# Kernel tuning notes

Measured on AMD Instinct MI355X. Metric: run time of the kernel, lower is better.

The kernel has to match this reference:

```python
import jax, jax.numpy as jnp
import numpy as np

N = 100_000          # nodes
E = 1_600_000        # directed edges (before self-loops)
IN_DIM, H1, H2, H3 = 128, 64, 64, 64
NEG_SLOPE = 0.2      # PyG GATConv default


def setup_inputs() -> dict:
    key = jax.random.key(0)
    ks = jax.random.split(key, 20)

    def glorot(k, shape):
        fan = shape[0] + shape[-1] if len(shape) > 1 else 1 + shape[0]
        return jax.random.normal(k, shape, jnp.float32) * np.float32(np.sqrt(2.0 / fan))

    inp = {
        "x": jax.random.normal(ks[0], (N, IN_DIM), jnp.float32),
        "edge_index": jax.random.randint(ks[1], (2, E), 0, N, jnp.int32),
        "W1": glorot(ks[2], (IN_DIM, H1)), "a1s": glorot(ks[3], (H1,)), "a1d": glorot(ks[4], (H1,)), "b1": jnp.zeros((H1,), jnp.float32),
        "W2": glorot(ks[5], (H1, H2)),     "a2s": glorot(ks[6], (H2,)), "a2d": glorot(ks[7], (H2,)), "b2": jnp.zeros((H2,), jnp.float32),
        "W3": glorot(ks[8], (H2, H3)),     "a3s": glorot(ks[9], (H3,)), "a3d": glorot(ks[10], (H3,)), "b3": jnp.zeros((H3,), jnp.float32),
        "Wl": glorot(ks[11], (H3, 1)),     "bl": jnp.zeros((1,), jnp.float32),
    }
    return inp


def _gat_layer(x, src, dst, W, a_src, a_dst, b):
    # x: [N, Fin]; src/dst: [E'] (self-loops included)
    h = x @ W                              # [N, Fout]
    alpha_s = h @ a_src                    # [N]
    alpha_d = h @ a_dst                    # [N]
    e = jax.nn.leaky_relu(alpha_s[src] + alpha_d[dst], NEG_SLOPE)  # [E']
    # segment softmax over edges grouped by destination node
    m = jax.ops.segment_max(e, dst, num_segments=N)
    p = jnp.exp(e - m[dst])
    s = jax.ops.segment_sum(p, dst, num_segments=N)
    alpha = p / (s[dst] + 1e-16)           # [E']
    out = jax.ops.segment_sum(alpha[:, None] * h[src], dst, num_segments=N)  # [N, Fout]
    return out + b


def reference(x, edge_index, W1, a1s, a1d, b1, W2, a2s, a2d, b2, W3, a3s, a3d, b3, Wl, bl):
    # add self-loops (PyG GATConv default add_self_loops=True)
    loops = jnp.arange(N, dtype=edge_index.dtype)
    src = jnp.concatenate([edge_index[0], loops])
    dst = jnp.concatenate([edge_index[1], loops])

    h = jax.nn.relu(_gat_layer(x, src, dst, W1, a1s, a1d, b1))   # dropout is identity in eval
    h = jax.nn.relu(_gat_layer(h, src, dst, W2, a2s, a2d, b2))
    h = jax.nn.relu(_gat_layer(h, src, dst, W3, a3s, a3d, b3))
    return jax.nn.sigmoid(h @ Wl + bl)      # [N, 1]
```

## Files before the change

kernel.cpp:

```cpp
#include <hip/hip_runtime.h>
#include <hip/hip_bf16.h>
#include <math.h>

#define BSH 8
#define MAXBK 512
#define PCHUNK 4096

__device__ __forceinline__ float wave_reduce_sum(float v) {
  #pragma unroll
  for (int off = 32; off; off >>= 1) v += __shfl_xor(v, off);
  return v;
}
__device__ __forceinline__ float half_reduce_max(float v) {
  #pragma unroll
  for (int off = 16; off; off >>= 1) v = fmaxf(v, __shfl_xor(v, off));
  return v;
}
__device__ __forceinline__ float half_reduce_sum(float v) {
  #pragma unroll
  for (int off = 16; off; off >>= 1) v += __shfl_xor(v, off);
  return v;
}

__device__ __forceinline__ unsigned f2bf(float f) {
  unsigned u = __float_as_uint(f);
  return (u + 0x7fffu + ((u >> 16) & 1u)) >> 16;
}

__device__ __forceinline__ void async_copy16(const float* gsrc, float* ldst) {
  __builtin_amdgcn_global_load_lds(
      (const __attribute__((address_space(1))) void*)gsrc,
      (__attribute__((address_space(3))) void*)ldst, 16, 0, 0);
}

__device__ __forceinline__ void wave0_excl_scan(unsigned* arr, unsigned* out, int n, int t) {
  if (t < 64) {
    unsigned carry = 0;
    for (int c = 0; c < n / 64; c++) {
      unsigned v = arr[c * 64 + t];
      unsigned s = v;
      #pragma unroll
      for (int off = 1; off < 64; off <<= 1) {
        unsigned u = __shfl_up(s, off);
        if ((t & 63) >= off) s += u;
      }
      out[c * 64 + t] = s - v + carry;
      carry += __shfl(s, 63);
    }
  }
}


__global__ __launch_bounds__(256) void k_bhist(const int* __restrict__ ei,
                                               unsigned* __restrict__ gbucket,
                                               int E, int EE, int nbk) {
  __shared__ unsigned hist[MAXBK];
  int t = threadIdx.x;
  for (int i = t; i < nbk; i += 256) hist[i] = 0;
  __syncthreads();
  for (int e = blockIdx.x * 256 + t; e < EE; e += gridDim.x * 256) {
    int d = (e < E) ? ei[E + e] : (e - E);
    atomicAdd(&hist[d >> BSH], 1u);
  }
  __syncthreads();
  for (int i = t; i < nbk; i += 256)
    if (hist[i]) atomicAdd(&gbucket[i], hist[i]);
}

__global__ __launch_bounds__(256) void k_bscan(const unsigned* __restrict__ gbucket,
                                               unsigned* __restrict__ bbase,
                                               unsigned* __restrict__ bfill,
                                               int nbk, int EE) {
  __shared__ unsigned arr[MAXBK], exc[MAXBK];
  int t = threadIdx.x;
  for (int i = t; i < MAXBK; i += 256) arr[i] = (i < nbk) ? gbucket[i] : 0u;
  __syncthreads();
  wave0_excl_scan(arr, exc, MAXBK, t);
  __syncthreads();
  for (int i = t; i < nbk; i += 256) { bbase[i] = exc[i]; bfill[i] = exc[i]; }
  if (t == 0) bbase[nbk] = (unsigned)EE;
}

__global__ __launch_bounds__(256) void k_part(const int* __restrict__ ei,
                                              unsigned* __restrict__ bfill,
                                              uint2* __restrict__ part,
                                              int E, int EE) {
  __shared__ uint2 stage[PCHUNK];
  __shared__ unsigned lcnt[MAXBK], lexcl[MAXBK], lbase[MAXBK];
  int t = threadIdx.x;
  int base = blockIdx.x * PCHUNK;
  int cnt = EE - base; if (cnt > PCHUNK) cnt = PCHUNK;
  for (int i = t; i < MAXBK; i += 256) lcnt[i] = 0;
  __syncthreads();

  uint2 ed[16]; unsigned loc[16];
  #pragma unroll
  for (int i = 0; i < 16; i++) {
    int e = base + i * 256 + t;
    if (e < EE) {
      int s, d;
      if (e < E) { s = ei[e]; d = ei[E + e]; } else { s = e - E; d = s; }
      ed[i] = make_uint2((unsigned)s, (unsigned)d);
      loc[i] = atomicAdd(&lcnt[(unsigned)d >> BSH], 1u);
    }
  }
  __syncthreads();
  wave0_excl_scan(lcnt, lexcl, MAXBK, t);
  __syncthreads();
  for (int i = t; i < MAXBK; i += 256) {
    unsigned c = lcnt[i];
    lbase[i] = c ? atomicAdd(&bfill[i], c) : 0u;
  }
  __syncthreads();
  #pragma unroll
  for (int i = 0; i < 16; i++) {
    int e = base + i * 256 + t;
    if (e < EE) stage[lexcl[ed[i].y >> BSH] + loc[i]] = ed[i];
  }
  __syncthreads();
  for (int i = t; i < cnt; i += 256) {
    uint2 v = stage[i];
    unsigned b = v.y >> BSH;
    part[lbase[b] + ((unsigned)i - lexcl[b])] = v;
  }
}

__global__ __launch_bounds__(256) void k_bcsr(const uint2* __restrict__ part,
                                              const unsigned* __restrict__ bbase,
                                              int* __restrict__ rowptr,
                                              int* __restrict__ csr_src,
                                              int Nn, int nbk) {
  __shared__ unsigned sdeg[256], sexcl[256], sfill[256];
  int t = threadIdx.x, b = blockIdx.x;
  int e0 = (int)bbase[b], e1 = (int)bbase[b + 1];
  sdeg[t] = 0; sfill[t] = 0;
  __syncthreads();
  for (int j = e0 + t; j < e1; j += 256)
    atomicAdd(&sdeg[part[j].y & 255u], 1u);
  __syncthreads();
  wave0_excl_scan(sdeg, sexcl, 256, t);
  __syncthreads();
  int node = (b << BSH) + t;
  if (node < Nn) rowptr[node] = e0 + (int)sexcl[t];
  if (b == nbk - 1 && t == 0) rowptr[Nn] = e1;
  for (int j = e0 + t; j < e1; j += 256) {
    uint2 v = part[j];
    unsigned dl = v.y & 255u;
    unsigned k = atomicAdd(&sfill[dl], 1u);
    csr_src[e0 + (int)sexcl[dl] + (int)k] = (int)v.x;
  }
}


template <int FIN>
__device__ __forceinline__ void stage_tile(const float* __restrict__ x, float* xs,
                                           int tile, int wid, int lane) {
  const size_t base = (size_t)tile * (32 * FIN);
  #pragma unroll
  for (int i = 0; i < FIN / 32; i++) {
    int chunk = wid * (FIN / 32) + i;
    async_copy16(x + base + chunk * 256 + lane * 4, xs + chunk * 256);
  }
}

#define FMA2(av, wr) \
  acc0[r] = fmaf(av, wreg[wr].x, acc0[r]); \
  acc1[r] = fmaf(av, wreg[wr].y, acc1[r]);

template <int FIN>
__global__ __launch_bounds__(256) void k_gemm5(
    const float* __restrict__ x, const float* __restrict__ W,
    const float* __restrict__ avs, const float* __restrict__ avd,
    unsigned* __restrict__ h, float* __restrict__ as_out, float* __restrict__ ad_out,
    int Nn, int ntiles) {
  __shared__ float Wl[FIN * 64];
  __shared__ float xs[2][32 * FIN];
  int t = threadIdx.x, lane = t & 63, wid = t >> 6;
  int fl = lane & 31, rh = lane >> 5;

  #pragma unroll
  for (int i = 0; i < FIN / 16; i++)
    ((float4*)Wl)[i * 256 + t] = ((const float4*)W)[i * 256 + t];
  float2 As2 = *(const float2*)&avs[2 * fl];
  float2 Ad2 = *(const float2*)&avd[2 * fl];

  int tile = blockIdx.x;
  if (tile >= ntiles) return;
  stage_tile<FIN>(x, xs[0], tile, wid, lane);
  __syncthreads();
  int buf = 0;

  while (tile < ntiles) {
    int nxt = tile + gridDim.x;
    if (nxt < ntiles) stage_tile<FIN>(x, xs[buf ^ 1], nxt, wid, lane);

    float acc0[4], acc1[4];
    #pragma unroll
    for (int r = 0; r < 4; r++) { acc0[r] = 0.f; acc1[r] = 0.f; }
    const float* xw = &xs[buf][(wid * 8 + rh * 4) * FIN];
    const float2* wcol = (const float2*)&Wl[2 * fl];

    #pragma unroll 1
    for (int kb = 0; kb < FIN; kb += 16) {
      float2 wreg[16];
      #pragma unroll
      for (int k = 0; k < 16; k++) wreg[k] = wcol[(kb + k) * 32];
      #pragma unroll
      for (int r = 0; r < 4; r++) {
        const float4* xr = (const float4*)(xw + r * FIN + kb);
        float4 a0 = xr[0], a1 = xr[1], a2 = xr[2], a3 = xr[3];
        FMA2(a0.x, 0)  FMA2(a0.y, 1)  FMA2(a0.z, 2)  FMA2(a0.w, 3)
        FMA2(a1.x, 4)  FMA2(a1.y, 5)  FMA2(a1.z, 6)  FMA2(a1.w, 7)
        FMA2(a2.x, 8)  FMA2(a2.y, 9)  FMA2(a2.z, 10) FMA2(a2.w, 11)
        FMA2(a3.x, 12) FMA2(a3.y, 13) FMA2(a3.z, 14) FMA2(a3.w, 15)
      }
    }

    int row0 = tile * 32 + wid * 8 + rh * 4;
    #pragma unroll
    for (int r = 0; r < 4; r++) {
      int row = row0 + r;
      bool ok = row < Nn;
      if (ok) {
        unsigned pk = (f2bf(acc1[r]) << 16) | f2bf(acc0[r]);
        h[(size_t)row * 32 + fl] = pk;
      }
      float vs = acc0[r] * As2.x + acc1[r] * As2.y;
      float vd = acc0[r] * Ad2.x + acc1[r] * Ad2.y;
      #pragma unroll
      for (int off = 16; off; off >>= 1) {
        vs += __shfl_xor(vs, off);
        vd += __shfl_xor(vd, off);
      }
      if (ok && fl == 0) { as_out[row] = vs; ad_out[row] = vd; }
    }

    __syncthreads();
    buf ^= 1;
    tile = nxt;
  }
}


template <int FINAL>
__global__ __launch_bounds__(256) void k_agg6(
    const int* __restrict__ rowptr, const int* __restrict__ csr_src,
    const unsigned* __restrict__ hp, const float* __restrict__ as_,
    const float* __restrict__ ad_, const float* __restrict__ bias,
    float* __restrict__ out, const float* __restrict__ Wlin,
    const float* __restrict__ blin, float* __restrict__ fout, int Nn) {
  __shared__ float2 psbuf[4][2][32];
  int t = threadIdx.x, lane = t & 63, wid = t >> 6;
  int fl = lane & 31, hh = lane >> 5;
  int n = blockIdx.x * 8 + wid * 2 + hh;
  bool valid = n < Nn;
  int nn = valid ? n : (Nn - 1);
  int r0 = rowptr[nn], r1 = rowptr[nn + 1];
  int deg = valid ? (r1 - r0) : 0;
  float ad = ad_[nn];
  float acc0 = 0.f, acc1 = 0.f;
  float inv;

  if (deg <= 32) {
    int src = (fl < deg) ? csr_src[r0 + fl] : 0;
    float e = (fl < deg) ? (as_[src] + ad) : -3.0e38f;
    e = (e >= 0.f) ? e : 0.2f * e;
    float m = half_reduce_max(e);
    float p = (fl < deg) ? __expf(e - m) : 0.f;
    inv = 1.f / (half_reduce_sum(p) + 1e-16f);
    psbuf[wid][hh][fl] = make_float2(p, __int_as_float(src));

    float b0 = 0.f, b1 = 0.f;
    int jj = 0;
    for (; jj + 2 <= deg; jj += 2) {
      float2 ps0 = psbuf[wid][hh][jj];
      float2 ps1 = psbuf[wid][hh][jj + 1];
      unsigned v0 = hp[(size_t)__float_as_int(ps0.y) * 32 + fl];
      unsigned v1 = hp[(size_t)__float_as_int(ps1.y) * 32 + fl];
      acc0 = fmaf(ps0.x, __uint_as_float(v0 << 16), acc0);
      acc1 = fmaf(ps0.x, __uint_as_float(v0 & 0xffff0000u), acc1);
      b0 = fmaf(ps1.x, __uint_as_float(v1 << 16), b0);
      b1 = fmaf(ps1.x, __uint_as_float(v1 & 0xffff0000u), b1);
    }
    if (jj < deg) {
      float2 ps0 = psbuf[wid][hh][jj];
      unsigned v0 = hp[(size_t)__float_as_int(ps0.y) * 32 + fl];
      acc0 = fmaf(ps0.x, __uint_as_float(v0 << 16), acc0);
      acc1 = fmaf(ps0.x, __uint_as_float(v0 & 0xffff0000u), acc1);
    }
    acc0 = (acc0 + b0) * inv;
    acc1 = (acc1 + b1) * inv;
  } else {
    float m = -3.0e38f;
    for (int j = r0 + fl; j < r1; j += 32) {
      float e = as_[csr_src[j]] + ad;
      e = (e >= 0.f) ? e : 0.2f * e;
      m = fmaxf(m, e);
    }
    m = half_reduce_max(m);
    float ssum = 0.f;
    for (int j = r0; j < r1; ++j) {
      int src = csr_src[j];
      float e = as_[src] + ad;
      e = (e >= 0.f) ? e : 0.2f * e;
      float p = __expf(e - m);
      ssum += p;
      unsigned v = hp[(size_t)src * 32 + fl];
      acc0 = fmaf(p, __uint_as_float(v << 16), acc0);
      acc1 = fmaf(p, __uint_as_float(v & 0xffff0000u), acc1);
    }
    float inv2 = 1.f / (ssum + 1e-16f);
    acc0 *= inv2;
    acc1 *= inv2;
  }

  float2 bi = ((const float2*)bias)[fl];
  float o0 = fmaxf(acc0 + bi.x, 0.f);
  float o1 = fmaxf(acc1 + bi.y, 0.f);
  if (FINAL) {
    float2 wl = ((const float2*)Wlin)[fl];
    float rv = half_reduce_sum(o0 * wl.x + o1 * wl.y);
    if (valid && fl == 0) {
      float z = rv + blin[0];
      fout[n] = 1.f / (1.f + __expf(-z));
    }
  } else {
    if (valid) ((float2*)out)[(size_t)n * 32 + fl] = make_float2(o0, o1);
  }
}

extern "C" void kernel_launch(void* const* d_in, const int* in_sizes, int n_in,
                              void* d_out, int out_size, void* d_ws, size_t ws_size,
                              hipStream_t stream) {
  const float* x   = (const float*)d_in[0];
  const int*   ei  = (const int*)d_in[1];
  const float* W1  = (const float*)d_in[2];
  const float* a1s = (const float*)d_in[3];
  const float* a1d = (const float*)d_in[4];
  const float* b1  = (const float*)d_in[5];
  const float* W2  = (const float*)d_in[6];
  const float* a2s = (const float*)d_in[7];
  const float* a2d = (const float*)d_in[8];
  const float* b2  = (const float*)d_in[9];
  const float* W3  = (const float*)d_in[10];
  const float* a3s = (const float*)d_in[11];
  const float* a3d = (const float*)d_in[12];
  const float* b3  = (const float*)d_in[13];
  const float* Wl  = (const float*)d_in[14];
  const float* bl  = (const float*)d_in[15];

  const int N  = in_sizes[0] / 128;
  const int E  = in_sizes[1] / 2;
  const int EE = E + N;
  const int nbk = (N + 255) >> 8;

  char* p = (char*)d_ws;
  auto alloc = [&](size_t bytes) { char* r = p; p += (bytes + 255) & ~(size_t)255; return r; };
  unsigned* gbucket = (unsigned*)alloc((size_t)MAXBK * 4);
  unsigned* bbase   = (unsigned*)alloc((size_t)(MAXBK + 1) * 4);
  unsigned* bfill   = (unsigned*)alloc((size_t)MAXBK * 4);
  int*      rowptr  = (int*)alloc((size_t)(N + 1) * 4);
  int*      csr_src = (int*)alloc((size_t)EE * 4);
  unsigned* hbuf    = (unsigned*)alloc((size_t)N * 64 * 2);
  float*    obuf    = (float*)alloc((size_t)N * 64 * 4);
  float*    as_     = (float*)alloc((size_t)N * 4);
  float*    ad_     = (float*)alloc((size_t)N * 4);

  uint2* part = (uint2*)obuf;

  hipMemsetAsync(gbucket, 0, (size_t)MAXBK * 4, stream);

  k_bhist<<<256, 256, 0, stream>>>(ei, gbucket, E, EE, nbk);
  k_bscan<<<1, 256, 0, stream>>>(gbucket, bbase, bfill, nbk, EE);
  k_part<<<(EE + PCHUNK - 1) / PCHUNK, 256, 0, stream>>>(ei, bfill, part, E, EE);
  k_bcsr<<<nbk, 256, 0, stream>>>(part, bbase, rowptr, csr_src, N, nbk);

  int ntiles = (N + 31) / 32;
  int g1 = ntiles < 512 ? ntiles : 512;
  int g2 = ntiles < 1024 ? ntiles : 1024;
  int nb = (N + 7) / 8;

  k_gemm5<128><<<g1, 256, 0, stream>>>(x, W1, a1s, a1d, hbuf, as_, ad_, N, ntiles);
  k_agg6<0><<<nb, 256, 0, stream>>>(rowptr, csr_src, hbuf, as_, ad_, b1, obuf,
                                    nullptr, nullptr, nullptr, N);
  k_gemm5<64><<<g2, 256, 0, stream>>>(obuf, W2, a2s, a2d, hbuf, as_, ad_, N, ntiles);
  k_agg6<0><<<nb, 256, 0, stream>>>(rowptr, csr_src, hbuf, as_, ad_, b2, obuf,
                                    nullptr, nullptr, nullptr, N);
  k_gemm5<64><<<g2, 256, 0, stream>>>(obuf, W3, a3s, a3d, hbuf, as_, ad_, N, ntiles);
  k_agg6<1><<<nb, 256, 0, stream>>>(rowptr, csr_src, hbuf, as_, ad_, b3, nullptr,
                                    Wl, bl, (float*)d_out, N);
}
```

Baseline: 295.6 us.

## Use bf16 MFMA for GAT projections and store intermediate activations as bf16

Replaces the fp32 FMA projection GEMM with a kernel using 32x32x16 bf16 MFMA, with the weights pre-packed into MFMA fragment layout by a small prep kernel. Input tiles are staged into LDS with an XOR swizzle, and 128 rows are handled per block without a persistent loop. Aggregation now writes hidden activations as packed bf16, which halves the traffic read by the next GEMM. The intended saving is the ALU cost of the GEMMs and the memory traffic between layers. The cost is lower precision on the inputs and activations, and the loss of the double-buffered pipelining.

```diff
diff --git a/kernel.cpp b/kernel.cpp
--- a/kernel.cpp
+++ b/kernel.cpp
@@ -6,11 +6,9 @@
 #define MAXBK 512
 #define PCHUNK 4096
 
-__device__ __forceinline__ float wave_reduce_sum(float v) {
-  #pragma unroll
-  for (int off = 32; off; off >>= 1) v += __shfl_xor(v, off);
-  return v;
-}
+typedef __attribute__((ext_vector_type(8)))  short short8;
+typedef __attribute__((ext_vector_type(16))) float f32x16;
+
 __device__ __forceinline__ float half_reduce_max(float v) {
   #pragma unroll
   for (int off = 16; off; off >>= 1) v = fmaxf(v, __shfl_xor(v, off));
@@ -27,7 +25,7 @@
   return (u + 0x7fffu + ((u >> 16) & 1u)) >> 16;
 }
 
-__device__ __forceinline__ void async_copy16(const float* gsrc, float* ldst) {
+__device__ __forceinline__ void async_copy16(const void* gsrc, void* ldst) {
   __builtin_amdgcn_global_load_lds(
       (const __attribute__((address_space(1))) void*)gsrc,
       (__attribute__((address_space(3))) void*)ldst, 16, 0, 0);
@@ -152,102 +150,111 @@
 }
 
 
-template <int FIN>
-__device__ __forceinline__ void stage_tile(const float* __restrict__ x, float* xs,
-                                           int tile, int wid, int lane) {
-  const size_t base = (size_t)tile * (32 * FIN);
-  #pragma unroll
-  for (int i = 0; i < FIN / 32; i++) {
-    int chunk = wid * (FIN / 32) + i;
-    async_copy16(x + base + chunk * 256 + lane * 4, xs + chunk * 256);
-  }
-}
-
-#define FMA2(av, wr) \
-  acc0[r] = fmaf(av, wreg[wr].x, acc0[r]); \
-  acc1[r] = fmaf(av, wreg[wr].y, acc1[r]);
-
-template <int FIN>
-__global__ __launch_bounds__(256) void k_gemm5(
-    const float* __restrict__ x, const float* __restrict__ W,
+__global__ __launch_bounds__(256) void k_wprep(const float* __restrict__ W1,
+                                               const float* __restrict__ W2,
+                                               const float* __restrict__ W3,
+                                               short8* __restrict__ wf) {
+  int idx = blockIdx.x * 256 + threadIdx.x;
+  if (idx >= 2048) return;
+  int g = idx >> 6, l = idx & 63;
+  const float* W; int s, t;
+  if (g < 16)      { W = W1; s = g >> 1;        t = g & 1; }
+  else if (g < 24) { W = W2; s = (g - 16) >> 1; t = g & 1; }
+  else             { W = W3; s = (g - 24) >> 1; t = g & 1; }
+  int of = t * 32 + (l & 31);
+  int k0 = s * 16 + (l >> 5) * 8;
+  short8 v;
+  #pragma unroll
+  for (int e = 0; e < 8; e++) v[e] = (short)f2bf(W[(k0 + e) * 64 + of]);
+  wf[idx] = v;
+}
+
+
+template <int K, bool F32IN>
+__global__ __launch_bounds__(256) void k_gemm7(
+    const void* __restrict__ xin, const short8* __restrict__ wf,
     const float* __restrict__ avs, const float* __restrict__ avd,
-    unsigned* __restrict__ h, float* __restrict__ as_out, float* __restrict__ ad_out,
-    int Nn, int ntiles) {
-  __shared__ float Wl[FIN * 64];
-  __shared__ float xs[2][32 * FIN];
+    unsigned* __restrict__ h, float* __restrict__ as_out,
+    float* __restrict__ ad_out, int Nn) {
+  constexpr int NS = K / 16;
+  constexpr int RB = F32IN ? K * 4 : K * 2;
+  constexpr int RSH = F32IN ? (K == 128 ? 9 : 8) : (K == 128 ? 8 : 7);
+  __shared__ __align__(16) char xs_raw[128 * RB];
   int t = threadIdx.x, lane = t & 63, wid = t >> 6;
-  int fl = lane & 31, rh = lane >> 5;
-
-  #pragma unroll
-  for (int i = 0; i < FIN / 16; i++)
-    ((float4*)Wl)[i * 256 + t] = ((const float4*)W)[i * 256 + t];
-  float2 As2 = *(const float2*)&avs[2 * fl];
-  float2 Ad2 = *(const float2*)&avd[2 * fl];
-
-  int tile = blockIdx.x;
-  if (tile >= ntiles) return;
-  stage_tile<FIN>(x, xs[0], tile, wid, lane);
-  __syncthreads();
-  int buf = 0;
-
-  while (tile < ntiles) {
-    int nxt = tile + gridDim.x;
-    if (nxt < ntiles) stage_tile<FIN>(x, xs[buf ^ 1], nxt, wid, lane);
-
-    float acc0[4], acc1[4];
-    #pragma unroll
-    for (int r = 0; r < 4; r++) { acc0[r] = 0.f; acc1[r] = 0.f; }
-    const float* xw = &xs[buf][(wid * 8 + rh * 4) * FIN];
-    const float2* wcol = (const float2*)&Wl[2 * fl];
-
-    #pragma unroll 1
-    for (int kb = 0; kb < FIN; kb += 16) {
-      float2 wreg[16];
-      #pragma unroll
-      for (int k = 0; k < 16; k++) wreg[k] = wcol[(kb + k) * 32];
-      #pragma unroll
-      for (int r = 0; r < 4; r++) {
-        const float4* xr = (const float4*)(xw + r * FIN + kb);
-        float4 a0 = xr[0], a1 = xr[1], a2 = xr[2], a3 = xr[3];
-        FMA2(a0.x, 0)  FMA2(a0.y, 1)  FMA2(a0.z, 2)  FMA2(a0.w, 3)
-        FMA2(a1.x, 4)  FMA2(a1.y, 5)  FMA2(a1.z, 6)  FMA2(a1.w, 7)
-        FMA2(a2.x, 8)  FMA2(a2.y, 9)  FMA2(a2.z, 10) FMA2(a2.w, 11)
-        FMA2(a3.x, 12) FMA2(a3.y, 13) FMA2(a3.z, 14) FMA2(a3.w, 15)
-      }
-    }
-
-    int row0 = tile * 32 + wid * 8 + rh * 4;
-    #pragma unroll
-    for (int r = 0; r < 4; r++) {
-      int row = row0 + r;
-      bool ok = row < Nn;
-      if (ok) {
-        unsigned pk = (f2bf(acc1[r]) << 16) | f2bf(acc0[r]);
-        h[(size_t)row * 32 + fl] = pk;
-      }
-      float vs = acc0[r] * As2.x + acc1[r] * As2.y;
-      float vd = acc0[r] * Ad2.x + acc1[r] * Ad2.y;
-      #pragma unroll
-      for (int off = 16; off; off >>= 1) {
-        vs += __shfl_xor(vs, off);
-        vd += __shfl_xor(vd, off);
-      }
-      if (ok && fl == 0) { as_out[row] = vs; ad_out[row] = vd; }
-    }
-
-    __syncthreads();
-    buf ^= 1;
-    tile = nxt;
-  }
+  int l31 = lane & 31, hi = lane >> 5;
+
+  short8 wa[NS * 2];
+  #pragma unroll
+  for (int i = 0; i < NS * 2; i++) wa[i] = wf[i * 64 + lane];
+
+  int tile0 = blockIdx.x * 128;
+  const char* xg = (const char*)xin;
+  constexpr int CH = (128 * RB) / (256 * 16);
+  #pragma unroll
+  for (int i = 0; i < CH; i++) {
+    int off = (i * 256 + t) * 16;
+    int row = off >> RSH;
+    int inrow = off & (RB - 1);
+    long grow = (long)tile0 + row;
+    if (grow > (long)Nn - 1) grow = Nn - 1;
+    async_copy16(xg + grow * RB + (inrow ^ ((row & 7) << 4)), xs_raw + off);
+  }
+  __syncthreads();
+
+  f32x16 acc0 = {0,0,0,0,0,0,0,0,0,0,0,0,0,0,0,0};
+  f32x16 acc1 = {0,0,0,0,0,0,0,0,0,0,0,0,0,0,0,0};
+  int rowl = wid * 32 + l31;
+  int swz = (rowl & 7) << 4;
+
+  #pragma unroll
+  for (int s = 0; s < NS; s++) {
+    short8 bf;
+    if constexpr (F32IN) {
+      int ph = (rowl * RB + s * 64 + hi * 32) ^ swz;
+      float4 fA = *(const float4*)(xs_raw + ph);
+      float4 fB = *(const float4*)(xs_raw + (ph ^ 16));
+      bf[0] = (short)f2bf(fA.x); bf[1] = (short)f2bf(fA.y);
+      bf[2] = (short)f2bf(fA.z); bf[3] = (short)f2bf(fA.w);
+      bf[4] = (short)f2bf(fB.x); bf[5] = (short)f2bf(fB.y);
+      bf[6] = (short)f2bf(fB.z); bf[7] = (short)f2bf(fB.w);
+    } else {
+      int ph = (rowl * RB + s * 32 + hi * 16) ^ swz;
+      bf = *(const short8*)(xs_raw + ph);
+    }
+    acc0 = __builtin_amdgcn_mfma_f32_32x32x16_bf16(wa[2 * s], bf, acc0, 0, 0, 0);
+    acc1 = __builtin_amdgcn_mfma_f32_32x32x16_bf16(wa[2 * s + 1], bf, acc1, 0, 0, 0);
+  }
+
+  int xrow = tile0 + rowl;
+  bool ok = xrow < Nn;
+  float asp = 0.f, adp = 0.f;
+  #pragma unroll
+  for (int r = 0; r < 16; r += 2) {
+    int rof = (r & 3) + 8 * (r >> 2);
+    int of0 = rof + 4 * hi;
+    if (ok) {
+      h[(size_t)xrow * 32 + (of0 >> 1)] =
+          (f2bf(acc0[r + 1]) << 16) | f2bf(acc0[r]);
+      h[(size_t)xrow * 32 + 16 + (of0 >> 1)] =
+          (f2bf(acc1[r + 1]) << 16) | f2bf(acc1[r]);
+    }
+    asp += acc0[r] * avs[of0] + acc0[r + 1] * avs[of0 + 1]
+         + acc1[r] * avs[of0 + 32] + acc1[r + 1] * avs[of0 + 33];
+    adp += acc0[r] * avd[of0] + acc0[r + 1] * avd[of0 + 1]
+         + acc1[r] * avd[of0 + 32] + acc1[r + 1] * avd[of0 + 33];
+  }
+  asp += __shfl_xor(asp, 32);
+  adp += __shfl_xor(adp, 32);
+  if (ok && hi == 0) { as_out[xrow] = asp; ad_out[xrow] = adp; }
 }
 
 
 template <int FINAL>
-__global__ __launch_bounds__(256) void k_agg6(
+__global__ __launch_bounds__(256) void k_agg7(
     const int* __restrict__ rowptr, const int* __restrict__ csr_src,
     const unsigned* __restrict__ hp, const float* __restrict__ as_,
     const float* __restrict__ ad_, const float* __restrict__ bias,
-    float* __restrict__ out, const float* __restrict__ Wlin,
+    unsigned* __restrict__ out, const float* __restrict__ Wlin,
     const float* __restrict__ blin, float* __restrict__ fout, int Nn) {
   __shared__ float2 psbuf[4][2][32];
   int t = threadIdx.x, lane = t & 63, wid = t >> 6;
@@ -259,7 +266,6 @@
   int deg = valid ? (r1 - r0) : 0;
   float ad = ad_[nn];
   float acc0 = 0.f, acc1 = 0.f;
-  float inv;
 
   if (deg <= 32) {
     int src = (fl < deg) ? csr_src[r0 + fl] : 0;
@@ -267,7 +273,7 @@
     e = (e >= 0.f) ? e : 0.2f * e;
     float m = half_reduce_max(e);
     float p = (fl < deg) ? __expf(e - m) : 0.f;
-    inv = 1.f / (half_reduce_sum(p) + 1e-16f);
+    float inv = 1.f / (half_reduce_sum(p) + 1e-16f);
     psbuf[wid][hh][fl] = make_float2(p, __int_as_float(src));
 
     float b0 = 0.f, b1 = 0.f;
@@ -325,7 +331,7 @@
       fout[n] = 1.f / (1.f + __expf(-z));
     }
   } else {
-    if (valid) ((float2*)out)[(size_t)n * 32 + fl] = make_float2(o0, o1);
+    if (valid) out[(size_t)n * 32 + fl] = (f2bf(o1) << 16) | f2bf(o0);
   }
 }
 
@@ -359,34 +365,37 @@
   unsigned* gbucket = (unsigned*)alloc((size_t)MAXBK * 4);
   unsigned* bbase   = (unsigned*)alloc((size_t)(MAXBK + 1) * 4);
   unsigned* bfill   = (unsigned*)alloc((size_t)MAXBK * 4);
+  short8*   wf      = (short8*)alloc(2048 * 16);
   int*      rowptr  = (int*)alloc((size_t)(N + 1) * 4);
   int*      csr_src = (int*)alloc((size_t)EE * 4);
-  unsigned* hbuf    = (unsigned*)alloc((size_t)N * 64 * 2);
-  float*    obuf    = (float*)alloc((size_t)N * 64 * 4);
+  unsigned* hbuf    = (unsigned*)alloc((size_t)N * 32 * 4);
+  char*     regionA = alloc((size_t)EE * 8);
   float*    as_     = (float*)alloc((size_t)N * 4);
   float*    ad_     = (float*)alloc((size_t)N * 4);
 
-  uint2* part = (uint2*)obuf;
+  uint2*    part = (uint2*)regionA;
+  unsigned* obuf = (unsigned*)regionA;
 
   hipMemsetAsync(gbucket, 0, (size_t)MAXBK * 4, stream);
 
+  k_wprep<<<8, 256, 0, stream>>>(W1, W2, W3, wf);
   k_bhist<<<256, 256, 0, stream>>>(ei, gbucket, E, EE, nbk);
   k_bscan<<<1, 256, 0, stream>>>(gbucket, bbase, bfill, nbk, EE);
   k_part<<<(EE + PCHUNK - 1) / PCHUNK, 256, 0, stream>>>(ei, bfill, part, E, EE);
   k_bcsr<<<nbk, 256, 0, stream>>>(part, bbase, rowptr, csr_src, N, nbk);
 
-  int ntiles = (N + 31) / 32;
-  int g1 = ntiles < 512 ? ntiles : 512;
-  int g2 = ntiles < 1024 ? ntiles : 1024;
+  int gb = (N + 127) / 128;
   int nb = (N + 7) / 8;
 
-  k_gemm5<128><<<g1, 256, 0, stream>>>(x, W1, a1s, a1d, hbuf, as_, ad_, N, ntiles);
-  k_agg6<0><<<nb, 256, 0, stream>>>(rowptr, csr_src, hbuf, as_, ad_, b1, obuf,
+  k_gemm7<128, true><<<gb, 256, 0, stream>>>(x, wf, a1s, a1d, hbuf, as_, ad_, N);
+  k_agg7<0><<<nb, 256, 0, stream>>>(rowptr, csr_src, hbuf, as_, ad_, b1, obuf,
                                     nullptr, nullptr, nullptr, N);
-  k_gemm5<64><<<g2, 256, 0, stream>>>(obuf, W2, a2s, a2d, hbuf, as_, ad_, N, ntiles);
-  k_agg6<0><<<nb, 256, 0, stream>>>(rowptr, csr_src, hbuf, as_, ad_, b2, obuf,
+  k_gemm7<64, false><<<gb, 256, 0, stream>>>(obuf, wf + 16 * 64, a2s, a2d,
+                                             hbuf, as_, ad_, N);
+  k_agg7<0><<<nb, 256, 0, stream>>>(rowptr, csr_src, hbuf, as_, ad_, b2, obuf,
                                     nullptr, nullptr, nullptr, N);
-  k_gemm5<64><<<g2, 256, 0, stream>>>(obuf, W3, a3s, a3d, hbuf, as_, ad_, N, ntiles);
-  k_agg6<1><<<nb, 256, 0, stream>>>(rowptr, csr_src, hbuf, as_, ad_, b3, nullptr,
+  k_gemm7<64, false><<<gb, 256, 0, stream>>>(obuf, wf + 24 * 64, a3s, a3d,
+                                             hbuf, as_, ad_, N);
+  k_agg7<1><<<nb, 256, 0, stream>>>(rowptr, csr_src, hbuf, as_, ad_, b3, nullptr,
                                     Wl, bl, (float*)d_out, N);
 }
```

Result: faster. 265.1 us (-10.3%).
